# Optimization experiments

Hardware: AMD Instinct MI355X
Metric: run time of the kernel (lower is better)

Reference implementation:

```python
import jax, jax.numpy as jnp
import numpy as np

H = 4096
HALF = H // 2          # 2048
COMP = H // 4          # 1024 (compression_ratio=4)
MEM = 32768
NUM_SAMPLES = 16384


def setup_inputs() -> dict:
    key = jax.random.key(0)
    ks = jax.random.split(key, 12)
    hidden_states = jax.random.normal(ks[0], (4, 2048, H), dtype=jnp.float32)
    memory = jax.random.normal(ks[1], (MEM, H), dtype=jnp.float32)
    idx = jax.random.randint(ks[2], (NUM_SAMPLES,), 0, MEM)
    eps = jax.random.normal(ks[3], (NUM_SAMPLES, COMP), dtype=jnp.float32)
    # encoder: H -> H/2 -> 2*COMP ; decoder: COMP -> H/2 -> H (fan-in scaled init)
    W1 = jax.random.normal(ks[4], (H, HALF), dtype=jnp.float32) / np.sqrt(H)
    b1 = jnp.zeros((HALF,), dtype=jnp.float32)
    W2 = jax.random.normal(ks[5], (HALF, 2 * COMP), dtype=jnp.float32) / np.sqrt(HALF)
    b2 = jnp.zeros((2 * COMP,), dtype=jnp.float32)
    Wd1 = jax.random.normal(ks[6], (COMP, HALF), dtype=jnp.float32) / np.sqrt(COMP)
    bd1 = jnp.zeros((HALF,), dtype=jnp.float32)
    Wd2 = jax.random.normal(ks[7], (HALF, H), dtype=jnp.float32) / np.sqrt(HALF)
    bd2 = jnp.zeros((H,), dtype=jnp.float32)
    return {"hidden_states": hidden_states, "memory": memory, "idx": idx, "eps": eps,
            "W1": W1, "b1": b1, "W2": W2, "b2": b2,
            "Wd1": Wd1, "bd1": bd1, "Wd2": Wd2, "bd2": bd2}


def reference(hidden_states, memory, idx, eps, W1, b1, W2, b2, Wd1, bd1, Wd2, bd2):
    B, T, Hd = hidden_states.shape
    flat = hidden_states.reshape(-1, Hd)
    n = min(flat.shape[0], memory.shape[0])
    # vectorized circular-buffer write (write_ptr starts at 0)
    pos = jnp.arange(n) % memory.shape[0]
    mem = memory.at[pos].set(flat[:n])
    # dream(): sample, VAE encode-reparam-decode, losses
    samples = mem[idx]                                   # [S, H]
    h = jax.nn.gelu(samples @ W1 + b1, approximate=False)
    enc = h @ W2 + b2                                    # [S, 2*COMP]
    mu, logvar = jnp.split(enc, 2, axis=-1)
    z = mu + jnp.exp(0.5 * logvar) * eps                 # [S, COMP]
    hd = jax.nn.gelu(z @ Wd1 + bd1, approximate=False)
    reconstructed = hd @ Wd2 + bd2                       # [S, H]
    recon_loss = jnp.mean((reconstructed - samples) ** 2)
    kl_loss = -0.5 * jnp.sum(1.0 + logvar - mu ** 2 - jnp.exp(logvar))
    return recon_loss + 0.001 * kl_loss
```

## Files before the change

### kernel.cpp

```cpp
#include <hip/hip_runtime.h>
#include <hip/hip_bf16.h>

using bf16 = __hip_bfloat16;
typedef __attribute__((ext_vector_type(16))) float f32x16;
typedef __attribute__((ext_vector_type(4)))  int   i32x4;
typedef __attribute__((ext_vector_type(8)))  int   i32x8;

#define DEVINL __device__ __forceinline__

#define ASCALE 16.0f
#define WSCALE 64.0f
#define SCALE_A_DW 0x7B7B7B7B
#define SCALE_B_DW 0x79797979

DEVINL unsigned char f2fp8(float x) {
    return (unsigned char)(__builtin_amdgcn_cvt_pk_fp8_f32(x, x, 0, 0) & 0xff);
}

DEVINL void gload_lds16(const void* g, void* l) {
    __builtin_amdgcn_global_load_lds(
        (const __attribute__((address_space(1))) void*)g,
        (__attribute__((address_space(3))) void*)l,
        16, 0, 0);
}

__global__ void init_acc(double* acc) {
    if (threadIdx.x < 2) acc[threadIdx.x] = 0.0;
}

__global__ void transpose_cast_fp8(const float* __restrict__ W,
                                   unsigned char* __restrict__ WT,
                                   int K, int N, int interleave) {
    __shared__ float tile[32][33];
    int n0 = blockIdx.x * 32, k0 = blockIdx.y * 32;
    int tx = threadIdx.x, ty0 = threadIdx.y;
#pragma unroll
    for (int i = 0; i < 4; ++i) {
        int ty = ty0 + i * 8;
        tile[ty][tx] = W[(size_t)(k0 + ty) * N + n0 + tx];
    }
    __syncthreads();
#pragma unroll
    for (int i = 0; i < 4; ++i) {
        int ty = ty0 + i * 8;
        int src = n0 + ty;
        int orow = interleave ? ((src < 1024) ? 2 * src : 2 * (src - 1024) + 1)
                              : src;
        WT[(size_t)orow * K + k0 + tx] = f2fp8(tile[tx][ty] * WSCALE);
    }
}

__global__ void gather_cast(const float* __restrict__ hidden,
                            const float* __restrict__ memory,
                            const int* __restrict__ idx,
                            unsigned char* __restrict__ samples8) {
    int s = blockIdx.x;
    int r = idx[s];
    const float* src = (r < 8192) ? hidden + (size_t)r * 4096
                                  : memory + (size_t)r * 4096;
    unsigned char* d8 = samples8 + (size_t)s * 4096;
#pragma unroll
    for (int c = threadIdx.x * 4; c < 4096; c += 1024) {
        float4 v = *(const float4*)(src + c);
        int w = __builtin_amdgcn_cvt_pk_fp8_f32(v.x * ASCALE, v.y * ASCALE, 0, 0);
        w = __builtin_amdgcn_cvt_pk_fp8_f32(v.z * ASCALE, v.w * ASCALE, w, 1);
        *(unsigned int*)(d8 + c) = (unsigned int)w;
    }
}

template <int EPI>
__global__ __launch_bounds__(256, 4)
void gemm128f8(const unsigned char* __restrict__ A,
               const unsigned char* __restrict__ BT,
               const float* __restrict__ bias, void* __restrict__ Cout,
               const unsigned char* __restrict__ S,
               const float* __restrict__ EPS, double* __restrict__ accum,
               int M, int N, int K, int MT) {
    __shared__ __align__(16) unsigned char lds[2][2][128 * 64];

    const int tid  = threadIdx.x;
    const int lane = tid & 63;
    const int wave = tid >> 6;
    const int wr   = wave >> 1;
    const int wc   = wave & 1;

    const int nwg  = gridDim.x;
    const int cpx  = nwg >> 3;
    const int work = (blockIdx.x & 7) * cpx + (blockIdx.x >> 3);
    const int ntile = work / MT;
    const int mtile = work - ntile * MT;
    const int m0 = mtile * 128;
    const int n0 = ntile * 128;

    const int nk = K >> 6;

    const int srow = tid >> 2;
    const int skb  = tid & 3;

    auto stage = [&](int buf, int kt) {
        const size_t kcol = (size_t)kt * 64;
#pragma unroll
        for (int mat = 0; mat < 2; ++mat) {
            const unsigned char* G = mat ? BT : A;
            const int base0 = mat ? n0 : m0;
#pragma unroll
            for (int j = 0; j < 2; ++j) {
                int row = j * 64 + srow;
                int sg  = skb ^ (row & 3);
                gload_lds16(G + (size_t)(base0 + row) * K + kcol + (size_t)sg * 16,
                            &lds[buf][mat][row * 64 + skb * 16]);
            }
        }
    };

    const int g32 = (lane >> 5);
    const int l31 = lane & 31;
    auto rdfrag = [&](const unsigned char* base, int row) -> i32x8 {
        const unsigned char* rp = base + row * 64;
        int r3 = row & 3;
        int s0 = g32 * 2;
        i32x4 lo = *(const i32x4*)(rp + (((s0    ) ^ r3) << 4));
        i32x4 hi = *(const i32x4*)(rp + (((s0 + 1) ^ r3) << 4));
        return __builtin_shufflevector(lo, hi, 0, 1, 2, 3, 4, 5, 6, 7);
    };

    f32x16 acc[2][2] = {};

    stage(0, 0);
    __syncthreads();
    int cur = 0;
    for (int t = 0; t < nk; ++t) {
        if (t + 1 < nk) stage(cur ^ 1, t + 1);
        i32x8 a0 = rdfrag(lds[cur][0], wr * 64 +  0 + l31);
        i32x8 a1 = rdfrag(lds[cur][0], wr * 64 + 32 + l31);
        i32x8 b0 = rdfrag(lds[cur][1], wc * 64 +  0 + l31);
        i32x8 b1 = rdfrag(lds[cur][1], wc * 64 + 32 + l31);
        acc[0][0] = __builtin_amdgcn_mfma_scale_f32_32x32x64_f8f6f4(
            a0, b0, acc[0][0], 0, 0, 0, SCALE_A_DW, 0, SCALE_B_DW);
        acc[0][1] = __builtin_amdgcn_mfma_scale_f32_32x32x64_f8f6f4(
            a0, b1, acc[0][1], 0, 0, 0, SCALE_A_DW, 0, SCALE_B_DW);
        acc[1][0] = __builtin_amdgcn_mfma_scale_f32_32x32x64_f8f6f4(
            a1, b0, acc[1][0], 0, 0, 0, SCALE_A_DW, 0, SCALE_B_DW);
        acc[1][1] = __builtin_amdgcn_mfma_scale_f32_32x32x64_f8f6f4(
            a1, b1, acc[1][1], 0, 0, 0, SCALE_A_DW, 0, SCALE_B_DW);
        __syncthreads();
        cur ^= 1;
    }

    float lsum = 0.f;
#pragma unroll
    for (int fr = 0; fr < 2; ++fr) {
#pragma unroll
        for (int fc = 0; fc < 2; ++fc) {
            int colg = n0 + wc * 64 + fc * 32 + l31;
            float bv;
            if (EPI == 2)
                bv = (colg & 1) ? bias[1024 + (colg >> 1)] : bias[colg >> 1];
            else
                bv = bias[colg];
#pragma unroll
            for (int reg = 0; reg < 16; ++reg) {
                int row = m0 + wr * 64 + fr * 32 +
                          (reg & 3) + 8 * (reg >> 2) + 4 * g32;
                float v = acc[fr][fc][reg] + bv;
                if (EPI == 0) {
                    float ge = 0.5f * v * (1.f + erff(v * 0.70710678118f));
                    ((unsigned char*)Cout)[(size_t)row * N + colg] =
                        f2fp8(ge * ASCALE);
                } else if (EPI == 2) {
                    float other = __shfl_xor(v, 1);
                    if ((lane & 1) == 0) {
                        float mu = v, lv = other;
                        float el = expf(lv);
                        size_t zi = (size_t)row * 1024 + (colg >> 1);
                        float zz = mu + sqrtf(el) * EPS[zi];
                        ((unsigned char*)Cout)[zi] = f2fp8(zz * ASCALE);
                        lsum += 1.f + lv - mu * mu - el;
                    }
                } else {
                    unsigned int sb = S[(size_t)row * N + colg];
                    float sv = __builtin_amdgcn_cvt_f32_fp8(sb, 0) * (1.0f / ASCALE);
                    float d = v - sv;
                    lsum += d * d;
                }
            }
        }
    }

    if (EPI == 2 || EPI == 3) {
        __shared__ float red[4];
        float v = lsum;
#pragma unroll
        for (int o = 32; o > 0; o >>= 1) v += __shfl_down(v, o);
        if (lane == 0) red[wave] = v;
        __syncthreads();
        if (tid == 0) {
            double t = (double)red[0] + (double)red[1] +
                       (double)red[2] + (double)red[3];
            atomicAdd(accum + (EPI == 2 ? 1 : 0), t);
        }
    }
}

__global__ void finalize_kernel(const double* __restrict__ acc,
                                float* __restrict__ out) {
    if (threadIdx.x == 0)
        out[0] = (float)(acc[0] * (1.0 / (16384.0 * 4096.0)) - 0.0005 * acc[1]);
}

extern "C" void kernel_launch(void* const* d_in, const int* in_sizes, int n_in,
                              void* d_out, int out_size, void* d_ws, size_t ws_size,
                              hipStream_t stream) {
    const float* hidden = (const float*)d_in[0];
    const float* memory = (const float*)d_in[1];
    const int*   idx    = (const int*)d_in[2];
    const float* eps    = (const float*)d_in[3];
    const float* W1     = (const float*)d_in[4];
    const float* b1     = (const float*)d_in[5];
    const float* W2     = (const float*)d_in[6];
    const float* b2     = (const float*)d_in[7];
    const float* Wd1    = (const float*)d_in[8];
    const float* bd1    = (const float*)d_in[9];
    const float* Wd2    = (const float*)d_in[10];
    const float* bd2    = (const float*)d_in[11];

    char* ws = (char*)d_ws;
    double* acc            = (double*)ws;
    unsigned char* s8      = (unsigned char*)(ws + 256);
    unsigned char* h8      = s8   + (size_t)16384 * 4096;
    unsigned char* z8      = h8   + (size_t)16384 * 2048;
    unsigned char* hd8     = z8   + (size_t)16384 * 1024;
    unsigned char* W1T     = hd8  + (size_t)16384 * 2048;
    unsigned char* W2T     = W1T  + (size_t)2048 * 4096;
    unsigned char* Wd1T    = W2T  + (size_t)2048 * 2048;
    unsigned char* Wd2T    = Wd1T + (size_t)2048 * 1024;

    init_acc<<<1, 64, 0, stream>>>(acc);

    dim3 tb(32, 8);
    transpose_cast_fp8<<<dim3(64, 128), tb, 0, stream>>>(W1, W1T, 4096, 2048, 0);
    transpose_cast_fp8<<<dim3(64, 64),  tb, 0, stream>>>(W2, W2T, 2048, 2048, 1);
    transpose_cast_fp8<<<dim3(64, 32),  tb, 0, stream>>>(Wd1, Wd1T, 1024, 2048, 0);
    transpose_cast_fp8<<<dim3(128, 64), tb, 0, stream>>>(Wd2, Wd2T, 2048, 4096, 0);

    gather_cast<<<16384, 256, 0, stream>>>(hidden, memory, idx, s8);

    gemm128f8<0><<<2048, 256, 0, stream>>>(s8, W1T, b1, h8, nullptr, nullptr,
                                           nullptr, 16384, 2048, 4096, 128);
    gemm128f8<2><<<2048, 256, 0, stream>>>(h8, W2T, b2, z8, nullptr, eps,
                                           acc, 16384, 2048, 2048, 128);
    gemm128f8<0><<<2048, 256, 0, stream>>>(z8, Wd1T, bd1, hd8, nullptr, nullptr,
                                           nullptr, 16384, 2048, 1024, 128);
    gemm128f8<3><<<4096, 256, 0, stream>>>(hd8, Wd2T, bd2, nullptr, s8,
                                           nullptr, acc, 16384, 4096, 2048, 128);

    finalize_kernel<<<1, 64, 0, stream>>>(acc, (float*)d_out);
}
```

Baseline: 692.8 us.

## Use two waves per 128x128 FP8 GEMM tile with 128x64 per-wave subtiles

Each GEMM workgroup drops from four waves to two, and each wave now computes a 128x64 slice (4x2 MFMA tiles) instead of a 64x64 slice. Each B fragment read from LDS is reused across four A fragments, which cuts LDS reads per MFMA. Staging loops are widened so 128 threads still fill the same LDS tiles. The cost is fewer waves per workgroup to hide latency, doubled accumulator register pressure, and a weaker launch-bounds occupancy hint.

```diff
diff --git a/kernel.cpp b/kernel.cpp
--- a/kernel.cpp
+++ b/kernel.cpp
@@ -69,7 +69,7 @@
 }
 
 template <int EPI>
-__global__ __launch_bounds__(256, 4)
+__global__ __launch_bounds__(128, 2)
 void gemm128f8(const unsigned char* __restrict__ A,
                const unsigned char* __restrict__ BT,
                const float* __restrict__ bias, void* __restrict__ Cout,
@@ -80,9 +80,7 @@
 
     const int tid  = threadIdx.x;
     const int lane = tid & 63;
-    const int wave = tid >> 6;
-    const int wr   = wave >> 1;
-    const int wc   = wave & 1;
+    const int wc   = tid >> 6;
 
     const int nwg  = gridDim.x;
     const int cpx  = nwg >> 3;
@@ -104,8 +102,8 @@
             const unsigned char* G = mat ? BT : A;
             const int base0 = mat ? n0 : m0;
 #pragma unroll
-            for (int j = 0; j < 2; ++j) {
-                int row = j * 64 + srow;
+            for (int j = 0; j < 4; ++j) {
+                int row = j * 32 + srow;
                 int sg  = skb ^ (row & 3);
                 gload_lds16(G + (size_t)(base0 + row) * K + kcol + (size_t)sg * 16,
                             &lds[buf][mat][row * 64 + skb * 16]);
@@ -124,35 +122,33 @@
         return __builtin_shufflevector(lo, hi, 0, 1, 2, 3, 4, 5, 6, 7);
     };
 
-    f32x16 acc[2][2] = {};
+    f32x16 acc[4][2] = {};
 
     stage(0, 0);
     __syncthreads();
     int cur = 0;
     for (int t = 0; t < nk; ++t) {
         if (t + 1 < nk) stage(cur ^ 1, t + 1);
-        i32x8 a0 = rdfrag(lds[cur][0], wr * 64 +  0 + l31);
-        i32x8 a1 = rdfrag(lds[cur][0], wr * 64 + 32 + l31);
         i32x8 b0 = rdfrag(lds[cur][1], wc * 64 +  0 + l31);
         i32x8 b1 = rdfrag(lds[cur][1], wc * 64 + 32 + l31);
-        acc[0][0] = __builtin_amdgcn_mfma_scale_f32_32x32x64_f8f6f4(
-            a0, b0, acc[0][0], 0, 0, 0, SCALE_A_DW, 0, SCALE_B_DW);
-        acc[0][1] = __builtin_amdgcn_mfma_scale_f32_32x32x64_f8f6f4(
-            a0, b1, acc[0][1], 0, 0, 0, SCALE_A_DW, 0, SCALE_B_DW);
-        acc[1][0] = __builtin_amdgcn_mfma_scale_f32_32x32x64_f8f6f4(
-            a1, b0, acc[1][0], 0, 0, 0, SCALE_A_DW, 0, SCALE_B_DW);
-        acc[1][1] = __builtin_amdgcn_mfma_scale_f32_32x32x64_f8f6f4(
-            a1, b1, acc[1][1], 0, 0, 0, SCALE_A_DW, 0, SCALE_B_DW);
+#pragma unroll
+        for (int mi = 0; mi < 4; ++mi) {
+            i32x8 a = rdfrag(lds[cur][0], mi * 32 + l31);
+            acc[mi][0] = __builtin_amdgcn_mfma_scale_f32_32x32x64_f8f6f4(
+                a, b0, acc[mi][0], 0, 0, 0, SCALE_A_DW, 0, SCALE_B_DW);
+            acc[mi][1] = __builtin_amdgcn_mfma_scale_f32_32x32x64_f8f6f4(
+                a, b1, acc[mi][1], 0, 0, 0, SCALE_A_DW, 0, SCALE_B_DW);
+        }
         __syncthreads();
         cur ^= 1;
     }
 
     float lsum = 0.f;
 #pragma unroll
-    for (int fr = 0; fr < 2; ++fr) {
-#pragma unroll
-        for (int fc = 0; fc < 2; ++fc) {
-            int colg = n0 + wc * 64 + fc * 32 + l31;
+    for (int mi = 0; mi < 4; ++mi) {
+#pragma unroll
+        for (int nj = 0; nj < 2; ++nj) {
+            int colg = n0 + wc * 64 + nj * 32 + l31;
             float bv;
             if (EPI == 2)
                 bv = (colg & 1) ? bias[1024 + (colg >> 1)] : bias[colg >> 1];
@@ -160,9 +156,8 @@
                 bv = bias[colg];
 #pragma unroll
             for (int reg = 0; reg < 16; ++reg) {
-                int row = m0 + wr * 64 + fr * 32 +
-                          (reg & 3) + 8 * (reg >> 2) + 4 * g32;
-                float v = acc[fr][fc][reg] + bv;
+                int row = m0 + mi * 32 + (reg & 3) + 8 * (reg >> 2) + 4 * g32;
+                float v = acc[mi][nj][reg] + bv;
                 if (EPI == 0) {
                     float ge = 0.5f * v * (1.f + erff(v * 0.70710678118f));
                     ((unsigned char*)Cout)[(size_t)row * N + colg] =
@@ -188,15 +183,14 @@
     }
 
     if (EPI == 2 || EPI == 3) {
-        __shared__ float red[4];
+        __shared__ float red[2];
         float v = lsum;
 #pragma unroll
         for (int o = 32; o > 0; o >>= 1) v += __shfl_down(v, o);
-        if (lane == 0) red[wave] = v;
+        if (lane == 0) red[wc] = v;
         __syncthreads();
         if (tid == 0) {
-            double t = (double)red[0] + (double)red[1] +
-                       (double)red[2] + (double)red[3];
+            double t = (double)red[0] + (double)red[1];
             atomicAdd(accum + (EPI == 2 ? 1 : 0), t);
         }
     }
@@ -245,13 +239,13 @@
 
     gather_cast<<<16384, 256, 0, stream>>>(hidden, memory, idx, s8);
 
-    gemm128f8<0><<<2048, 256, 0, stream>>>(s8, W1T, b1, h8, nullptr, nullptr,
+    gemm128f8<0><<<2048, 128, 0, stream>>>(s8, W1T, b1, h8, nullptr, nullptr,
                                            nullptr, 16384, 2048, 4096, 128);
-    gemm128f8<2><<<2048, 256, 0, stream>>>(h8, W2T, b2, z8, nullptr, eps,
+    gemm128f8<2><<<2048, 128, 0, stream>>>(h8, W2T, b2, z8, nullptr, eps,
                                            acc, 16384, 2048, 2048, 128);
-    gemm128f8<0><<<2048, 256, 0, stream>>>(z8, Wd1T, bd1, hd8, nullptr, nullptr,
+    gemm128f8<0><<<2048, 128, 0, stream>>>(z8, Wd1T, bd1, hd8, nullptr, nullptr,
                                            nullptr, 16384, 2048, 1024, 128);
-    gemm128f8<3><<<4096, 256, 0, stream>>>(hd8, Wd2T, bd2, nullptr, s8,
+    gemm128f8<3><<<4096, 128, 0, stream>>>(hd8, Wd2T, bd2, nullptr, s8,
                                            nullptr, acc, 16384, 4096, 2048, 128);
 
     finalize_kernel<<<1, 64, 0, stream>>>(acc, (float*)d_out);
```

Result: slower. 870.3 us (+25.6%).
